# Kernel optimization log

Hardware: AMD Instinct MI355X
Metric: run time of the kernel (lower is better)

## Reference

```python
import jax, jax.numpy as jnp
import numpy as np

N = 4096
IN_F = 512
OUT_F = 64
HEADS = 4
ALPHA = 0.2  # leaky relu slope
NEG_INF = -9e15


def setup_inputs() -> dict:
    key = jax.random.key(0)
    k1, k2, k3, k4 = jax.random.split(key, 4)
    x = jax.random.normal(k1, (N, IN_F), dtype=jnp.float32)
    adj = jax.random.randint(k2, (N, N), 0, 2, dtype=jnp.int32)
    # xavier-uniform-like init for params
    limW = float(np.sqrt(6.0 / (IN_F + OUT_F * HEADS)))
    W = jax.random.uniform(k3, (IN_F, OUT_F * HEADS), dtype=jnp.float32, minval=-limW, maxval=limW)
    lima = float(np.sqrt(6.0 / (2 * OUT_F + 1)))
    a = jax.random.uniform(k4, (2 * OUT_F, 1), dtype=jnp.float32, minval=-lima, maxval=lima)
    return {"x": x, "adj": adj, "W": W, "a": a}


def reference(x, adj, W, a):
    # h: [N, H, F]
    h = (x @ W).reshape(N, HEADS, OUT_F)
    a_src = a[:OUT_F, 0]   # [F]
    a_dst = a[OUT_F:, 0]   # [F]
    s = jnp.einsum("nhf,f->nh", h, a_src)  # source-node score [N, H]
    t = jnp.einsum("nhf,f->nh", h, a_dst)  # dest-node score   [N, H]
    # e[i, j, k] = leaky_relu(s[i,k] + t[j,k]) -> [N, N, H]
    e = jax.nn.leaky_relu(s[:, None, :] + t[None, :, :], negative_slope=ALPHA)
    mask = (adj > 0)[:, :, None]  # [N, N, 1]
    e = jnp.where(mask, e, NEG_INF)
    attn = jax.nn.softmax(e, axis=1)  # softmax over neighbors j
    # weighted aggregation per head: [N, H, F]
    h_prime = jnp.einsum("ijh,jhf->ihf", attn, h)
    return h_prime.reshape(N, HEADS * OUT_F)
```

## Files before the change

### kernel.cpp

```cpp
#include <hip/hip_runtime.h>
#include <hip/hip_bf16.h>


#define NN 4096
#define KF 512
#define NF 256

typedef __attribute__((ext_vector_type(8))) short bf16x8;
typedef __attribute__((ext_vector_type(4))) short s16x4;
typedef __attribute__((ext_vector_type(4))) float f32x4;

union AB8 { bf16x8 v; short2 h[4]; short s[8]; int4 i4; };
union ST4 { s16x4 v; short2 h[2]; };
union I64 { long v; int i[2]; };

__device__ __forceinline__ short f2bf(float f) {
    union { float f; unsigned u; } v; v.f = f;
    unsigned r = v.u + 0x7fffu + ((v.u >> 16) & 1u);
    return (short)(r >> 16);
}
__device__ __forceinline__ short2 pkbf(float a, float b) {
    __hip_bfloat162 t = __float22bfloat162_rn(make_float2(a, b));
    union { __hip_bfloat162 v; short2 s; } u; u.v = t;
    return u.s;
}
__device__ __forceinline__ int pkfp8x4(float a, float b, float c, float d) {
    int p = __builtin_amdgcn_cvt_pk_fp8_f32(a, b, 0, false);
    p     = __builtin_amdgcn_cvt_pk_fp8_f32(c, d, p, true);
    return p;
}

__global__ __launch_bounds__(256) void stage1(const float* __restrict__ x,
                                              const float* __restrict__ W,
                                              short* __restrict__ xF,
                                              short* __restrict__ WtF) {
    if (blockIdx.x < 1024) {
        const int lane = threadIdx.x & 63, wv = threadIdx.x >> 6;
        const int i = blockIdx.x * 4 + wv;
        const float4* xp = (const float4*)(x + (size_t)i * KF + lane * 8);
        float4 xa = xp[0], xb = xp[1];
        ST4 o0, o1;
        o0.h[0] = pkbf(xa.x, xa.y); o0.h[1] = pkbf(xa.z, xa.w);
        o1.h[0] = pkbf(xb.x, xb.y); o1.h[1] = pkbf(xb.z, xb.w);
        const int kblk = lane >> 2, qk = lane & 3;
        const int jgrp = i >> 4, r = i & 15;
        short* dst = xF + ((size_t)(kblk * 256 + jgrp) * 64 + qk * 16 + r) * 8;
        *(s16x4*)dst = o0.v;
        *(s16x4*)(dst + 4) = o1.v;
    } else {
        int tid = (blockIdx.x - 1024) * 256 + threadIdx.x;
        int l = tid & 63, nt = (tid >> 6) & 3, hd = (tid >> 8) & 3, kblk = tid >> 10;
        int q = l >> 4, r = l & 15;
        int col = hd * 64 + nt * 16 + r;
        int k0 = kblk * 32 + q * 8;
        AB8 o;
        #pragma unroll
        for (int e = 0; e < 8; e++) o.s[e] = f2bf(W[(k0 + e) * NF + col]);
        *(bf16x8*)(WtF + (size_t)tid * 8) = o.v;
    }
}

__global__ __launch_bounds__(256) void stage2(const short* __restrict__ xF,
                                              const short* __restrict__ WtF,
                                              const float* __restrict__ a,
                                              const int* __restrict__ adj,
                                              unsigned char* __restrict__ VtF8,
                                              float* __restrict__ ipk,
                                              float2* __restrict__ jpk,
                                              unsigned* __restrict__ pT) {
    if (blockIdx.x < 256) {
        const int lane = threadIdx.x & 63, wv = threadIdx.x >> 6;
        const int q = lane >> 4, r = lane & 15;
        const int jb32 = blockIdx.x >> 1, ch = blockIdx.x & 1;
        const int rg = wv >> 1, hd = ch * 2 + (wv & 1);
        const int jgrp = jb32 * 2 + rg;

        const short* ap = xF  + ((size_t)jgrp * 64 + lane) * 8;
        const short* wp = WtF + ((size_t)(hd * 4) * 64 + lane) * 8;

        f32x4 acc[4] = {};
        #pragma unroll
        for (int kblk = 0; kblk < 16; kblk++) {
            bf16x8 av = *(const bf16x8*)(ap + (size_t)kblk * 256 * 512);
            const short* w = wp + (size_t)kblk * 16 * 512;
            #pragma unroll
            for (int nt = 0; nt < 4; nt++) {
                bf16x8 bv = *(const bf16x8*)(w + nt * 512);
                acc[nt] = __builtin_amdgcn_mfma_f32_16x16x32_bf16(av, bv, acc[nt], 0, 0, 0);
            }
        }
        const int base = rg * 16 + q * 4;
        const int qa = base >> 3, e0 = base & 7;
        #pragma unroll
        for (int nt = 0; nt < 4; nt++) {
            size_t slot = (size_t)(((jb32 * 4 + hd) * 4 + nt) * 64 + qa * 16 + r);
            *(int*)(VtF8 + slot * 8 + e0) = pkfp8x4(acc[nt][0], acc[nt][1], acc[nt][2], acc[nt][3]);
        }
        float as[4], at[4];
        #pragma unroll
        for (int nt = 0; nt < 4; nt++) { as[nt] = a[nt * 16 + r]; at[nt] = a[64 + nt * 16 + r]; }
        f32x4 sp = {}, tp = {};
        #pragma unroll
        for (int nt = 0; nt < 4; nt++)
            #pragma unroll
            for (int reg = 0; reg < 4; reg++) {
                sp[reg] += acc[nt][reg] * as[nt];
                tp[reg] += acc[nt][reg] * at[nt];
            }
        #pragma unroll
        for (int d = 1; d < 16; d <<= 1)
            #pragma unroll
            for (int reg = 0; reg < 4; reg++) {
                sp[reg] += __shfl_xor(sp[reg], d, 64);
                tp[reg] += __shfl_xor(tp[reg], d, 64);
            }
        if (r == 0) {
            #pragma unroll
            for (int reg = 0; reg < 4; reg++) {
                int j = jb32 * 32 + rg * 16 + q * 4 + reg;
                ipk[hd * NN + j] = __expf(-0.8f * sp[reg]);
                jpk[hd * NN + j] = make_float2(__expf(tp[reg]), __expf(0.2f * tp[reg]));
            }
        }
    } else {
        int gw   = ((blockIdx.x - 256) * 256 + threadIdx.x) >> 6;
        int lane = threadIdx.x & 63;
        int i = gw >> 4, seg = gw & 15;
        const int* ap = adj + (size_t)i * NN + seg * 256 + lane;
        unsigned long long b0 = __ballot(ap[0]   != 0);
        unsigned long long b1 = __ballot(ap[64]  != 0);
        unsigned long long b2 = __ballot(ap[128] != 0);
        unsigned long long b3 = __ballot(ap[192] != 0);
        if (lane == 0) {
            *(uint4*)(pT + ((size_t)(seg * 2    ) * NN + i) * 4) =
                make_uint4((unsigned)b0, (unsigned)(b0 >> 32), (unsigned)b1, (unsigned)(b1 >> 32));
            *(uint4*)(pT + ((size_t)(seg * 2 + 1) * NN + i) * 4) =
                make_uint4((unsigned)b2, (unsigned)(b2 >> 32), (unsigned)b3, (unsigned)(b3 >> 32));
        }
    }
}

__global__ __launch_bounds__(512, 8)
void gat_attn(const uint4* __restrict__ pT4, const float* __restrict__ ipk,
              const float* __restrict__ jpkf, const unsigned char* __restrict__ VtF8,
              float* __restrict__ out) {
    const int lane = threadIdx.x & 63, js = threadIdx.x >> 6;
    const int hd = blockIdx.x & 3, itile = blockIdx.x >> 2;
    const int q = lane >> 4, r = lane & 15;
    const int i0 = itile * 16, i = i0 + r;
    const float ci = ipk[hd * NN + i];
    const int qs = q * 8;

    f32x4 acc[5] = {};
    const long ones = 0x3838383838383838L;

    const int it0 = js * 16;
    const float* jp = jpkf + (size_t)hd * NN * 2 + 2 * ((it0 << 5) + qs);
    const long*  vp = (const long*)(VtF8 + (size_t)(it0 * 16 + hd * 4) * 512) + lane;
    const uint4* prow = pT4 + (size_t)(js * 4) * NN + i;

    auto consume = [&](unsigned w, float4 ja, float4 jb, float4 jc, float4 jd,
                       long v0, long v1, long v2, long v3) {
        float p0 = (w & 1u)   ? fmaxf(ja.x, ci * ja.y) : 0.f;
        float p1 = (w & 2u)   ? fmaxf(ja.z, ci * ja.w) : 0.f;
        float p2 = (w & 4u)   ? fmaxf(jb.x, ci * jb.y) : 0.f;
        float p3 = (w & 8u)   ? fmaxf(jb.z, ci * jb.w) : 0.f;
        float p4 = (w & 16u)  ? fmaxf(jc.x, ci * jc.y) : 0.f;
        float p5 = (w & 32u)  ? fmaxf(jc.z, ci * jc.w) : 0.f;
        float p6 = (w & 64u)  ? fmaxf(jd.x, ci * jd.y) : 0.f;
        float p7 = (w & 128u) ? fmaxf(jd.z, ci * jd.w) : 0.f;
        I64 af;
        af.i[0] = pkfp8x4(p0, p1, p2, p3);
        af.i[1] = pkfp8x4(p4, p5, p6, p7);
        acc[0] = __builtin_amdgcn_mfma_f32_16x16x32_fp8_fp8(af.v, v0, acc[0], 0, 0, 0);
        acc[1] = __builtin_amdgcn_mfma_f32_16x16x32_fp8_fp8(af.v, v1, acc[1], 0, 0, 0);
        acc[2] = __builtin_amdgcn_mfma_f32_16x16x32_fp8_fp8(af.v, v2, acc[2], 0, 0, 0);
        acc[3] = __builtin_amdgcn_mfma_f32_16x16x32_fp8_fp8(af.v, v3, acc[3], 0, 0, 0);
        acc[4] = __builtin_amdgcn_mfma_f32_16x16x32_fp8_fp8(af.v, ones, acc[4], 0, 0, 0);
    };

    #pragma unroll 1
    for (int g = 0; g < 4; g++) {
        uint4 wg = prow[(size_t)g * NN];
        #pragma unroll
        for (int u = 0; u < 4; u++) {
            unsigned w = (u == 0 ? wg.x : u == 1 ? wg.y : u == 2 ? wg.z : wg.w) >> qs;
            const float4* jpv = (const float4*)jp;
            consume(w, jpv[0], jpv[1], jpv[2], jpv[3], vp[0], vp[64], vp[128], vp[192]);
            jp += 64; vp += 1024;
        }
    }

    __shared__ float sacc[7][5][64][4];
    if (js > 0) {
        #pragma unroll
        for (int t = 0; t < 5; t++)
            *(f32x4*)&sacc[js - 1][t][lane][0] = acc[t];
    }
    __syncthreads();
    if (js == 0) {
        #pragma unroll 1
        for (int gg = 0; gg < 7; gg++)
            #pragma unroll
            for (int t = 0; t < 5; t++) {
                f32x4 o = *(const f32x4*)&sacc[gg][t][lane][0];
                acc[t][0] += o[0]; acc[t][1] += o[1];
                acc[t][2] += o[2]; acc[t][3] += o[3];
            }
        #pragma unroll
        for (int reg = 0; reg < 4; reg++) {
            float inv = 1.f / acc[4][reg];
            int row = i0 + q * 4 + reg;
            #pragma unroll
            for (int t = 0; t < 4; t++)
                out[(size_t)row * NF + hd * 64 + t * 16 + r] = acc[t][reg] * inv;
        }
    }
}

extern "C" void kernel_launch(void* const* d_in, const int* in_sizes, int n_in,
                              void* d_out, int out_size, void* d_ws, size_t ws_size,
                              hipStream_t stream) {
    const float* x   = (const float*)d_in[0];
    const int*   adj = (const int*)d_in[1];
    const float* W   = (const float*)d_in[2];
    const float* a   = (const float*)d_in[3];
    float* out = (float*)d_out;

    char* ws = (char*)d_ws;
    short*         xF   = (short*)ws;
    short*         WtF  = (short*)(ws + 4194304);
    unsigned char* VtF8 = (unsigned char*)(ws + 4456448);
    unsigned*      pT   = (unsigned*)(ws + 5505024);
    float*         ipk  = (float*)(ws + 7602176);
    float2*        jpk  = (float2*)(ws + 7667712);

    stage1  <<<1088, 256, 0, stream>>>(x, W, xF, WtF);
    stage2  <<<16640, 256, 0, stream>>>(xF, WtF, a, adj, VtF8, ipk, jpk, pT);
    gat_attn<<<1024, 512, 0, stream>>>((const uint4*)pT, ipk, (const float*)jpk, VtF8, out);
}
```

Baseline: 141.7 us.

## Process two 16-row i-tiles per block to reuse loaded V and j-scores

Each attention block now handles 32 destination rows instead of 16, so every j-score and fp8 V load feeds two sets of MFMAs and the grid is halved. Masking changes from per-element selects to packing all probabilities and ANDing with a shared-memory byte-mask lookup table. This doubles the accumulator registers and shared reduction buffer and lowers the occupancy hint from 8 to 4, which may reduce latency hiding.

```diff
diff --git a/kernel.cpp b/kernel.cpp
--- a/kernel.cpp
+++ b/kernel.cpp
@@ -140,61 +140,75 @@
     }
 }
 
-__global__ __launch_bounds__(512, 8)
+__global__ __launch_bounds__(512, 4)
 void gat_attn(const uint4* __restrict__ pT4, const float* __restrict__ ipk,
               const float* __restrict__ jpkf, const unsigned char* __restrict__ VtF8,
               float* __restrict__ out) {
     const int lane = threadIdx.x & 63, js = threadIdx.x >> 6;
-    const int hd = blockIdx.x & 3, itile = blockIdx.x >> 2;
+    const int hd = blockIdx.x & 3, it32 = blockIdx.x >> 2;
     const int q = lane >> 4, r = lane & 15;
-    const int i0 = itile * 16, i = i0 + r;
-    const float ci = ipk[hd * NN + i];
+    const int i0 = it32 * 32, ia = i0 + r;
+    const float cia = ipk[hd * NN + ia];
+    const float cib = ipk[hd * NN + ia + 16];
     const int qs = q * 8;
 
-    f32x4 acc[5] = {};
+    __shared__ unsigned lut[16];
+    __shared__ float sacc[7][10][64][4];
+    if (threadIdx.x < 16) {
+        unsigned m01 = (threadIdx.x * 0x204081u) & 0x01010101u;
+        lut[threadIdx.x] = m01 * 0xFFu;
+    }
+    __syncthreads();
+
+    f32x4 acc[10] = {};
     const long ones = 0x3838383838383838L;
 
     const int it0 = js * 16;
     const float* jp = jpkf + (size_t)hd * NN * 2 + 2 * ((it0 << 5) + qs);
     const long*  vp = (const long*)(VtF8 + (size_t)(it0 * 16 + hd * 4) * 512) + lane;
-    const uint4* prow = pT4 + (size_t)(js * 4) * NN + i;
-
-    auto consume = [&](unsigned w, float4 ja, float4 jb, float4 jc, float4 jd,
-                       long v0, long v1, long v2, long v3) {
-        float p0 = (w & 1u)   ? fmaxf(ja.x, ci * ja.y) : 0.f;
-        float p1 = (w & 2u)   ? fmaxf(ja.z, ci * ja.w) : 0.f;
-        float p2 = (w & 4u)   ? fmaxf(jb.x, ci * jb.y) : 0.f;
-        float p3 = (w & 8u)   ? fmaxf(jb.z, ci * jb.w) : 0.f;
-        float p4 = (w & 16u)  ? fmaxf(jc.x, ci * jc.y) : 0.f;
-        float p5 = (w & 32u)  ? fmaxf(jc.z, ci * jc.w) : 0.f;
-        float p6 = (w & 64u)  ? fmaxf(jd.x, ci * jd.y) : 0.f;
-        float p7 = (w & 128u) ? fmaxf(jd.z, ci * jd.w) : 0.f;
+    const uint4* prow = pT4 + (size_t)(js * 4) * NN + ia;
+
+    auto iset = [&](unsigned w, float ci, f32x4* ac,
+                    float4 ja, float4 jb, float4 jc, float4 jd,
+                    long v0, long v1, long v2, long v3) {
+        float p0 = fmaxf(ja.x, ci * ja.y);
+        float p1 = fmaxf(ja.z, ci * ja.w);
+        float p2 = fmaxf(jb.x, ci * jb.y);
+        float p3 = fmaxf(jb.z, ci * jb.w);
+        float p4 = fmaxf(jc.x, ci * jc.y);
+        float p5 = fmaxf(jc.z, ci * jc.w);
+        float p6 = fmaxf(jd.x, ci * jd.y);
+        float p7 = fmaxf(jd.z, ci * jd.w);
         I64 af;
-        af.i[0] = pkfp8x4(p0, p1, p2, p3);
-        af.i[1] = pkfp8x4(p4, p5, p6, p7);
-        acc[0] = __builtin_amdgcn_mfma_f32_16x16x32_fp8_fp8(af.v, v0, acc[0], 0, 0, 0);
-        acc[1] = __builtin_amdgcn_mfma_f32_16x16x32_fp8_fp8(af.v, v1, acc[1], 0, 0, 0);
-        acc[2] = __builtin_amdgcn_mfma_f32_16x16x32_fp8_fp8(af.v, v2, acc[2], 0, 0, 0);
-        acc[3] = __builtin_amdgcn_mfma_f32_16x16x32_fp8_fp8(af.v, v3, acc[3], 0, 0, 0);
-        acc[4] = __builtin_amdgcn_mfma_f32_16x16x32_fp8_fp8(af.v, ones, acc[4], 0, 0, 0);
+        af.i[0] = pkfp8x4(p0, p1, p2, p3) & (int)lut[w & 15u];
+        af.i[1] = pkfp8x4(p4, p5, p6, p7) & (int)lut[(w >> 4) & 15u];
+        ac[0] = __builtin_amdgcn_mfma_f32_16x16x32_fp8_fp8(af.v, v0, ac[0], 0, 0, 0);
+        ac[1] = __builtin_amdgcn_mfma_f32_16x16x32_fp8_fp8(af.v, v1, ac[1], 0, 0, 0);
+        ac[2] = __builtin_amdgcn_mfma_f32_16x16x32_fp8_fp8(af.v, v2, ac[2], 0, 0, 0);
+        ac[3] = __builtin_amdgcn_mfma_f32_16x16x32_fp8_fp8(af.v, v3, ac[3], 0, 0, 0);
+        ac[4] = __builtin_amdgcn_mfma_f32_16x16x32_fp8_fp8(af.v, ones, ac[4], 0, 0, 0);
     };
 
     #pragma unroll 1
     for (int g = 0; g < 4; g++) {
-        uint4 wg = prow[(size_t)g * NN];
+        uint4 wga = prow[(size_t)g * NN];
+        uint4 wgb = prow[(size_t)g * NN + 16];
         #pragma unroll
         for (int u = 0; u < 4; u++) {
-            unsigned w = (u == 0 ? wg.x : u == 1 ? wg.y : u == 2 ? wg.z : wg.w) >> qs;
+            unsigned wa = (u == 0 ? wga.x : u == 1 ? wga.y : u == 2 ? wga.z : wga.w) >> qs;
+            unsigned wb = (u == 0 ? wgb.x : u == 1 ? wgb.y : u == 2 ? wgb.z : wgb.w) >> qs;
             const float4* jpv = (const float4*)jp;
-            consume(w, jpv[0], jpv[1], jpv[2], jpv[3], vp[0], vp[64], vp[128], vp[192]);
+            float4 ja = jpv[0], jb = jpv[1], jc = jpv[2], jd = jpv[3];
+            long v0 = vp[0], v1 = vp[64], v2 = vp[128], v3 = vp[192];
+            iset(wa, cia, acc,     ja, jb, jc, jd, v0, v1, v2, v3);
+            iset(wb, cib, acc + 5, ja, jb, jc, jd, v0, v1, v2, v3);
             jp += 64; vp += 1024;
         }
     }
 
-    __shared__ float sacc[7][5][64][4];
     if (js > 0) {
         #pragma unroll
-        for (int t = 0; t < 5; t++)
+        for (int t = 0; t < 10; t++)
             *(f32x4*)&sacc[js - 1][t][lane][0] = acc[t];
     }
     __syncthreads();
@@ -202,18 +216,21 @@
         #pragma unroll 1
         for (int gg = 0; gg < 7; gg++)
             #pragma unroll
-            for (int t = 0; t < 5; t++) {
+            for (int t = 0; t < 10; t++) {
                 f32x4 o = *(const f32x4*)&sacc[gg][t][lane][0];
                 acc[t][0] += o[0]; acc[t][1] += o[1];
                 acc[t][2] += o[2]; acc[t][3] += o[3];
             }
         #pragma unroll
         for (int reg = 0; reg < 4; reg++) {
-            float inv = 1.f / acc[4][reg];
-            int row = i0 + q * 4 + reg;
-            #pragma unroll
-            for (int t = 0; t < 4; t++)
-                out[(size_t)row * NF + hd * 64 + t * 16 + r] = acc[t][reg] * inv;
+            float inva = 1.f / acc[4][reg];
+            float invb = 1.f / acc[9][reg];
+            int rowa = i0 + q * 4 + reg;
+            #pragma unroll
+            for (int t = 0; t < 4; t++) {
+                out[(size_t)rowa * NF + hd * 64 + t * 16 + r] = acc[t][reg] * inva;
+                out[(size_t)(rowa + 16) * NF + hd * 64 + t * 16 + r] = acc[t + 5][reg] * invb;
+            }
         }
     }
 }
@@ -237,5 +254,5 @@
 
     stage1  <<<1088, 256, 0, stream>>>(x, W, xF, WtF);
     stage2  <<<16640, 256, 0, stream>>>(xF, WtF, a, adj, VtF8, ipk, jpk, pT);
-    gat_attn<<<1024, 512, 0, stream>>>((const uint4*)pT, ipk, (const float*)jpk, VtF8, out);
-}
+    gat_attn<<<512, 512, 0, stream>>>((const uint4*)pT, ipk, (const float*)jpk, VtF8, out);
+}
```

Result: faster. 127.9 us (-9.8%).
